# Optimization experiments

Hardware: AMD Instinct MI355X
Metric: run time of the kernel (lower is better)

The kernel has to match this reference:

```python
import jax, jax.numpy as jnp
import numpy as np

N_NODES = 50000
N_EDGES = 500000
D_NODE = 128
D_EDGE = 128
D_HID = 512
D_OUT = 128


def setup_inputs() -> dict:
    key = jax.random.key(0)
    ks = jax.random.split(key, 6)
    x = jax.random.normal(ks[0], (N_NODES, D_NODE), dtype=jnp.float32)
    edge_index = jax.random.randint(ks[1], (2, N_EDGES), 0, N_NODES, dtype=jnp.int64 if jax.config.jax_enable_x64 else jnp.int32)
    edge_attr = jax.random.normal(ks[2], (N_EDGES, D_EDGE), dtype=jnp.float32)
    cin = 2 * D_NODE + D_EDGE
    W1 = jax.random.normal(ks[3], (cin, D_HID), dtype=jnp.float32) * (1.0 / np.sqrt(cin))
    b1 = jnp.zeros((D_HID,), dtype=jnp.float32)
    W2 = jax.random.normal(ks[4], (D_HID, D_OUT), dtype=jnp.float32) * (1.0 / np.sqrt(D_HID))
    b2 = jnp.zeros((D_OUT,), dtype=jnp.float32)
    return {"x": x, "edge_index": edge_index, "edge_attr": edge_attr,
            "W1": W1, "b1": b1, "W2": W2, "b2": b2}


def reference(x, edge_index, edge_attr, W1, b1, W2, b2):
    row, col = edge_index[0], edge_index[1]
    source = x[row]            # [E, d_node] gather
    target = x[col]            # [E, d_node] gather
    out = jnp.concatenate([source, target, edge_attr], axis=1)  # [E, 2*d_node + d_edge]
    h = jax.nn.relu(out @ W1 + b1)   # [E, d_hid]
    return h @ W2 + b2               # [E, d_out]
```

## Files before the change

### kernel.cpp

```cpp
#include <hip/hip_runtime.h>

#define E_TOTAL 500000
#define N_NODES 50000
#define DN 128
#define CIN 384
#define DH 512
#define DOUT 128
#define MT 64
#define NTILE 7813
#define LDA 392
#define LDH 520

typedef short short8 __attribute__((ext_vector_type(8)));
typedef float f32x4 __attribute__((ext_vector_type(4)));

__device__ inline short f2bf(float f) {
    unsigned int u = __float_as_uint(f);
    u = (u + 0x7FFFu + ((u >> 16) & 1u)) >> 16;
    return (short)u;
}

__global__ void prep_weights(const float* __restrict__ w1,
                             const float* __restrict__ w2,
                             short* __restrict__ w1t,
                             short* __restrict__ w2t) {
    __shared__ float t[32][33];
    int b = blockIdx.x;
    const float* src; short* dst; int R, C, tr, tc;
    if (b < 192) { src = w1; dst = w1t; R = 384; C = 512; tr = b >> 4; tc = b & 15; }
    else { b -= 192; src = w2; dst = w2t; R = 512; C = 128; tr = b >> 2; tc = b & 3; }
    int lx = threadIdx.x & 31, ly = threadIdx.x >> 5;
#pragma unroll
    for (int p = 0; p < 4; p++) {
        int r = tr * 32 + p * 8 + ly;
        t[p * 8 + ly][lx] = src[(size_t)r * C + tc * 32 + lx];
    }
    __syncthreads();
#pragma unroll
    for (int p = 0; p < 4; p++) {
        int c = tc * 32 + p * 8 + ly;
        dst[(size_t)c * R + tr * 32 + lx] = f2bf(t[lx][p * 8 + ly]);
    }
}

__global__ void cvt_x(const float* __restrict__ x, short* __restrict__ xb) {
    int i = blockIdx.x * 256 + threadIdx.x;
    const float4* s = reinterpret_cast<const float4*>(x) + (size_t)i * 2;
    float4 a = s[0], b = s[1];
    short8 p;
    p[0] = f2bf(a.x); p[1] = f2bf(a.y); p[2] = f2bf(a.z); p[3] = f2bf(a.w);
    p[4] = f2bf(b.x); p[5] = f2bf(b.y); p[6] = f2bf(b.z); p[7] = f2bf(b.w);
    reinterpret_cast<short8*>(xb)[i] = p;
}

__global__ __launch_bounds__(512, 4) void edge_mlp(
        const short* __restrict__ xb,
        const float* __restrict__ xf,
        const int* __restrict__ ei,
        const float* __restrict__ ea,
        const float* __restrict__ b1,
        const float* __restrict__ b2,
        const short* __restrict__ w1t,
        const short* __restrict__ w2t,
        float* __restrict__ out) {
    __shared__ short sBuf[MT * LDH];
    __shared__ int sIdx[2][MT];
    short (*sA)[LDA] = (short (*)[LDA])sBuf;
    short (*sH)[LDH] = (short (*)[LDH])sBuf;

    const int tid = threadIdx.x;
    const int wave = tid >> 6;
    const int lane = tid & 63;
    const int l16 = lane & 15;
    const int quad = lane >> 4;
    const int lane32 = tid & 31;
    const int g = tid >> 5;
    const int e0 = blockIdx.x * MT;

    if (tid < 2 * MT) {
        int rr = tid >> 6, r = tid & 63;
        int e = e0 + r; e = e < E_TOTAL ? e : E_TOTAL - 1;
        sIdx[rr][r] = ei[rr * E_TOTAL + e];
    }
    __syncthreads();

    short4 gx[8];
    float4 ge[4];
    if (xb) {
#pragma unroll
        for (int j = 0; j < 4; j++) {
            int r = g + 16 * j;
            gx[j]     = reinterpret_cast<const short4*>(xb + (size_t)sIdx[0][r] * DN)[lane32];
            gx[4 + j] = reinterpret_cast<const short4*>(xb + (size_t)sIdx[1][r] * DN)[lane32];
            int e = e0 + r; e = e < E_TOTAL ? e : E_TOTAL - 1;
            ge[j] = reinterpret_cast<const float4*>(ea + (size_t)e * DN)[lane32];
        }
    } else {
#pragma unroll
        for (int j = 0; j < 4; j++) {
            int r = g + 16 * j;
            float4 v0 = reinterpret_cast<const float4*>(xf + (size_t)sIdx[0][r] * DN)[lane32];
            float4 v1 = reinterpret_cast<const float4*>(xf + (size_t)sIdx[1][r] * DN)[lane32];
            short4 p0, p1;
            p0.x = f2bf(v0.x); p0.y = f2bf(v0.y); p0.z = f2bf(v0.z); p0.w = f2bf(v0.w);
            p1.x = f2bf(v1.x); p1.y = f2bf(v1.y); p1.z = f2bf(v1.z); p1.w = f2bf(v1.w);
            gx[j] = p0; gx[4 + j] = p1;
            int e = e0 + r; e = e < E_TOTAL ? e : E_TOTAL - 1;
            ge[j] = reinterpret_cast<const float4*>(ea + (size_t)e * DN)[lane32];
        }
    }
    const short* base1 = w1t + (size_t)(wave * 64 + l16) * CIN + quad * 8;
    short8 bb[4];
#pragma unroll
    for (int nt = 0; nt < 4; nt++)
        bb[nt] = *reinterpret_cast<const short8*>(base1 + nt * 16 * CIN);
#pragma unroll
    for (int j = 0; j < 4; j++) {
        int r = g + 16 * j;
        *reinterpret_cast<short4*>(&sA[r][0 * DN + lane32 * 4]) = gx[j];
        *reinterpret_cast<short4*>(&sA[r][1 * DN + lane32 * 4]) = gx[4 + j];
        short4 p;
        p.x = f2bf(ge[j].x); p.y = f2bf(ge[j].y); p.z = f2bf(ge[j].z); p.w = f2bf(ge[j].w);
        *reinterpret_cast<short4*>(&sA[r][2 * DN + lane32 * 4]) = p;
    }
    __syncthreads();

    f32x4 acc[4][4] = {};
    for (int k = 0; k < CIN; k += 32) {
        short8 bn[4];
        if (k + 32 < CIN) {
#pragma unroll
            for (int nt = 0; nt < 4; nt++)
                bn[nt] = *reinterpret_cast<const short8*>(base1 + nt * 16 * CIN + k + 32);
        }
        short8 a[4];
#pragma unroll
        for (int mt = 0; mt < 4; mt++)
            a[mt] = *reinterpret_cast<const short8*>(&sA[mt * 16 + l16][k + quad * 8]);
#pragma unroll
        for (int nt = 0; nt < 4; nt++)
#pragma unroll
            for (int mt = 0; mt < 4; mt++)
                acc[nt][mt] = __builtin_amdgcn_mfma_f32_16x16x32_bf16(bb[nt], a[mt], acc[nt][mt], 0, 0, 0);
        if (k + 32 < CIN) {
#pragma unroll
            for (int nt = 0; nt < 4; nt++) bb[nt] = bn[nt];
        }
    }

    const short* base2 = w2t + (size_t)(wave * 16 + l16) * DH + quad * 8;
    short8 bw = *reinterpret_cast<const short8*>(base2);
    float4 b1v[4];
#pragma unroll
    for (int nt = 0; nt < 4; nt++)
        b1v[nt] = *reinterpret_cast<const float4*>(&b1[wave * 64 + nt * 16 + quad * 4]);

    __syncthreads();

#pragma unroll
    for (int nt = 0; nt < 4; nt++) {
#pragma unroll
        for (int mt = 0; mt < 4; mt++) {
            short4 p;
            p.x = f2bf(fmaxf(acc[nt][mt][0] + b1v[nt].x, 0.0f));
            p.y = f2bf(fmaxf(acc[nt][mt][1] + b1v[nt].y, 0.0f));
            p.z = f2bf(fmaxf(acc[nt][mt][2] + b1v[nt].z, 0.0f));
            p.w = f2bf(fmaxf(acc[nt][mt][3] + b1v[nt].w, 0.0f));
            *reinterpret_cast<short4*>(&sH[mt * 16 + l16][wave * 64 + nt * 16 + quad * 4]) = p;
        }
    }
    __syncthreads();

    f32x4 acc2[4] = {};
#pragma unroll
    for (int kk = 0; kk < 16; kk++) {
        short8 bn = bw;
        if (kk < 15) bn = *reinterpret_cast<const short8*>(base2 + (kk + 1) * 32);
        short8 hf[4];
#pragma unroll
        for (int mt = 0; mt < 4; mt++)
            hf[mt] = *reinterpret_cast<const short8*>(&sH[mt * 16 + l16][kk * 32 + quad * 8]);
#pragma unroll
        for (int mt = 0; mt < 4; mt++)
            acc2[mt] = __builtin_amdgcn_mfma_f32_16x16x32_bf16(bw, hf[mt], acc2[mt], 0, 0, 0);
        bw = bn;
    }
    float4 b2v = *reinterpret_cast<const float4*>(&b2[wave * 16 + quad * 4]);
#pragma unroll
    for (int mt = 0; mt < 4; mt++) {
        int e = e0 + mt * 16 + l16;
        if (e < E_TOTAL) {
            float4 o;
            o.x = acc2[mt][0] + b2v.x;
            o.y = acc2[mt][1] + b2v.y;
            o.z = acc2[mt][2] + b2v.z;
            o.w = acc2[mt][3] + b2v.w;
            *reinterpret_cast<float4*>(&out[(size_t)e * DOUT + wave * 16 + quad * 4]) = o;
        }
    }
}

extern "C" void kernel_launch(void* const* d_in, const int* in_sizes, int n_in,
                              void* d_out, int out_size, void* d_ws, size_t ws_size,
                              hipStream_t stream) {
    const float* x  = (const float*)d_in[0];
    const int*   ei = (const int*)d_in[1];
    const float* ea = (const float*)d_in[2];
    const float* W1 = (const float*)d_in[3];
    const float* b1 = (const float*)d_in[4];
    const float* W2 = (const float*)d_in[5];
    const float* b2 = (const float*)d_in[6];
    float* outp = (float*)d_out;

    short* w1t = (short*)d_ws;
    short* w2t = w1t + DH * CIN;
    prep_weights<<<256, 256, 0, stream>>>(W1, W2, w1t, w2t);

    const size_t wt_bytes = (size_t)(DH * CIN + DOUT * DH) * 2;
    const size_t xb_bytes = (size_t)N_NODES * DN * 2;
    short* xb = nullptr;
    if (ws_size >= wt_bytes + xb_bytes) {
        xb = w2t + DOUT * DH;
        cvt_x<<<3125, 256, 0, stream>>>(x, xb);
    }
    edge_mlp<<<NTILE, 512, 0, stream>>>(xb, x, ei, ea, b1, b2, w1t, w2t, outp);
}
```

Before: 964.1 us.

## Double edge tile to 128 with 1024 threads, XOR-swizzled LDS, staged coalesced output

Doubles the edge tile per block to 128 rows and the block to 16 waves. Each wave now owns 32 hidden columns over 128 rows in GEMM1, and in GEMM2 16 output columns over a 64-row half. This halves how often each W1 fragment is fetched from global/L2 per edge. LDS padding is replaced by an XOR swizzle to avoid bank conflicts, and results are staged through LDS so each row is written with coalesced stores. The cost is 128KB of shared memory per block, which limits occupancy to one block per CU, plus extra barriers.

New measurement: 941.7 us. 1.02x faster.

```diff
diff --git a/kernel.cpp b/kernel.cpp
--- a/kernel.cpp
+++ b/kernel.cpp
@@ -6,10 +6,11 @@
 #define CIN 384
 #define DH 512
 #define DOUT 128
-#define MT 64
-#define NTILE 7813
-#define LDA 392
-#define LDH 520
+#define MT 128
+#define NTILE 3907
+#define SA_ROWB 768
+#define SH_ROWB 1024
+#define SO_LD 132
 
 typedef short short8 __attribute__((ext_vector_type(8)));
 typedef float f32x4 __attribute__((ext_vector_type(4)));
@@ -53,7 +54,7 @@
     reinterpret_cast<short8*>(xb)[i] = p;
 }
 
-__global__ __launch_bounds__(512, 4) void edge_mlp(
+__global__ __launch_bounds__(1024, 4) void edge_mlp(
         const short* __restrict__ xb,
         const float* __restrict__ xf,
         const int* __restrict__ ei,
@@ -63,10 +64,9 @@
         const short* __restrict__ w1t,
         const short* __restrict__ w2t,
         float* __restrict__ out) {
-    __shared__ short sBuf[MT * LDH];
+    __shared__ short sBuf[65536];
     __shared__ int sIdx[2][MT];
-    short (*sA)[LDA] = (short (*)[LDA])sBuf;
-    short (*sH)[LDH] = (short (*)[LDH])sBuf;
+    char* sb = (char*)sBuf;
 
     const int tid = threadIdx.x;
     const int wave = tid >> 6;
@@ -75,10 +75,11 @@
     const int quad = lane >> 4;
     const int lane32 = tid & 31;
     const int g = tid >> 5;
+    const int xorv = (l16 & 7) << 4;
     const int e0 = blockIdx.x * MT;
 
     if (tid < 2 * MT) {
-        int rr = tid >> 6, r = tid & 63;
+        int rr = tid >> 7, r = tid & 127;
         int e = e0 + r; e = e < E_TOTAL ? e : E_TOTAL - 1;
         sIdx[rr][r] = ei[rr * E_TOTAL + e];
     }
@@ -89,7 +90,7 @@
     if (xb) {
 #pragma unroll
         for (int j = 0; j < 4; j++) {
-            int r = g + 16 * j;
+            int r = g + 32 * j;
             gx[j]     = reinterpret_cast<const short4*>(xb + (size_t)sIdx[0][r] * DN)[lane32];
             gx[4 + j] = reinterpret_cast<const short4*>(xb + (size_t)sIdx[1][r] * DN)[lane32];
             int e = e0 + r; e = e < E_TOTAL ? e : E_TOTAL - 1;
@@ -98,7 +99,7 @@
     } else {
 #pragma unroll
         for (int j = 0; j < 4; j++) {
-            int r = g + 16 * j;
+            int r = g + 32 * j;
             float4 v0 = reinterpret_cast<const float4*>(xf + (size_t)sIdx[0][r] * DN)[lane32];
             float4 v1 = reinterpret_cast<const float4*>(xf + (size_t)sIdx[1][r] * DN)[lane32];
             short4 p0, p1;
@@ -109,64 +110,72 @@
             ge[j] = reinterpret_cast<const float4*>(ea + (size_t)e * DN)[lane32];
         }
     }
-    const short* base1 = w1t + (size_t)(wave * 64 + l16) * CIN + quad * 8;
-    short8 bb[4];
-#pragma unroll
-    for (int nt = 0; nt < 4; nt++)
+    const short* base1 = w1t + (size_t)(wave * 32 + l16) * CIN + quad * 8;
+    short8 bb[2];
+#pragma unroll
+    for (int nt = 0; nt < 2; nt++)
         bb[nt] = *reinterpret_cast<const short8*>(base1 + nt * 16 * CIN);
 #pragma unroll
     for (int j = 0; j < 4; j++) {
-        int r = g + 16 * j;
-        *reinterpret_cast<short4*>(&sA[r][0 * DN + lane32 * 4]) = gx[j];
-        *reinterpret_cast<short4*>(&sA[r][1 * DN + lane32 * 4]) = gx[4 + j];
+        int r = g + 32 * j;
+        int rx = (r & 7) << 4;
+        char* row = sb + r * SA_ROWB;
+        *reinterpret_cast<short4*>(row + (( 0 * 256 + lane32 * 8) ^ rx)) = gx[j];
+        *reinterpret_cast<short4*>(row + (( 1 * 256 + lane32 * 8) ^ rx)) = gx[4 + j];
         short4 p;
         p.x = f2bf(ge[j].x); p.y = f2bf(ge[j].y); p.z = f2bf(ge[j].z); p.w = f2bf(ge[j].w);
-        *reinterpret_cast<short4*>(&sA[r][2 * DN + lane32 * 4]) = p;
-    }
-    __syncthreads();
-
-    f32x4 acc[4][4] = {};
+        *reinterpret_cast<short4*>(row + (( 2 * 256 + lane32 * 8) ^ rx)) = p;
+    }
+    __syncthreads();
+
+    f32x4 acc[2][8] = {};
     for (int k = 0; k < CIN; k += 32) {
-        short8 bn[4];
+        short8 bn[2];
         if (k + 32 < CIN) {
 #pragma unroll
-            for (int nt = 0; nt < 4; nt++)
+            for (int nt = 0; nt < 2; nt++)
                 bn[nt] = *reinterpret_cast<const short8*>(base1 + nt * 16 * CIN + k + 32);
         }
-        short8 a[4];
-#pragma unroll
-        for (int mt = 0; mt < 4; mt++)
-            a[mt] = *reinterpret_cast<const short8*>(&sA[mt * 16 + l16][k + quad * 8]);
-#pragma unroll
-        for (int nt = 0; nt < 4; nt++)
-#pragma unroll
-            for (int mt = 0; mt < 4; mt++)
+        short8 a[8];
+#pragma unroll
+        for (int mt = 0; mt < 8; mt++) {
+            int m = mt * 16 + l16;
+            a[mt] = *reinterpret_cast<const short8*>(
+                sb + m * SA_ROWB + ((2 * k + quad * 16) ^ xorv));
+        }
+#pragma unroll
+        for (int nt = 0; nt < 2; nt++)
+#pragma unroll
+            for (int mt = 0; mt < 8; mt++)
                 acc[nt][mt] = __builtin_amdgcn_mfma_f32_16x16x32_bf16(bb[nt], a[mt], acc[nt][mt], 0, 0, 0);
         if (k + 32 < CIN) {
 #pragma unroll
-            for (int nt = 0; nt < 4; nt++) bb[nt] = bn[nt];
-        }
-    }
-
-    const short* base2 = w2t + (size_t)(wave * 16 + l16) * DH + quad * 8;
+            for (int nt = 0; nt < 2; nt++) bb[nt] = bn[nt];
+        }
+    }
+
+    const int wn = wave & 7, half = wave >> 3;
+    const short* base2 = w2t + (size_t)(wn * 16 + l16) * DH + quad * 8;
     short8 bw = *reinterpret_cast<const short8*>(base2);
-    float4 b1v[4];
-#pragma unroll
-    for (int nt = 0; nt < 4; nt++)
-        b1v[nt] = *reinterpret_cast<const float4*>(&b1[wave * 64 + nt * 16 + quad * 4]);
-
-    __syncthreads();
-
-#pragma unroll
-    for (int nt = 0; nt < 4; nt++) {
-#pragma unroll
-        for (int mt = 0; mt < 4; mt++) {
+    float4 b1v[2];
+#pragma unroll
+    for (int nt = 0; nt < 2; nt++)
+        b1v[nt] = *reinterpret_cast<const float4*>(&b1[wave * 32 + nt * 16 + quad * 4]);
+
+    __syncthreads();
+
+#pragma unroll
+    for (int nt = 0; nt < 2; nt++) {
+#pragma unroll
+        for (int mt = 0; mt < 8; mt++) {
+            int m = mt * 16 + l16;
             short4 p;
             p.x = f2bf(fmaxf(acc[nt][mt][0] + b1v[nt].x, 0.0f));
             p.y = f2bf(fmaxf(acc[nt][mt][1] + b1v[nt].y, 0.0f));
             p.z = f2bf(fmaxf(acc[nt][mt][2] + b1v[nt].z, 0.0f));
             p.w = f2bf(fmaxf(acc[nt][mt][3] + b1v[nt].w, 0.0f));
-            *reinterpret_cast<short4*>(&sH[mt * 16 + l16][wave * 64 + nt * 16 + quad * 4]) = p;
+            *reinterpret_cast<short4*>(
+                sb + m * SH_ROWB + ((wave * 64 + nt * 32 + quad * 8) ^ xorv)) = p;
         }
     }
     __syncthreads();
@@ -178,24 +187,37 @@
         if (kk < 15) bn = *reinterpret_cast<const short8*>(base2 + (kk + 1) * 32);
         short8 hf[4];
 #pragma unroll
-        for (int mt = 0; mt < 4; mt++)
-            hf[mt] = *reinterpret_cast<const short8*>(&sH[mt * 16 + l16][kk * 32 + quad * 8]);
+        for (int mt = 0; mt < 4; mt++) {
+            int m = half * 64 + mt * 16 + l16;
+            hf[mt] = *reinterpret_cast<const short8*>(
+                sb + m * SH_ROWB + ((kk * 64 + quad * 16) ^ xorv));
+        }
 #pragma unroll
         for (int mt = 0; mt < 4; mt++)
             acc2[mt] = __builtin_amdgcn_mfma_f32_16x16x32_bf16(bw, hf[mt], acc2[mt], 0, 0, 0);
         bw = bn;
     }
-    float4 b2v = *reinterpret_cast<const float4*>(&b2[wave * 16 + quad * 4]);
+    float4 b2v = *reinterpret_cast<const float4*>(&b2[wn * 16 + quad * 4]);
+    __syncthreads();
+
+    float (*sO)[SO_LD] = (float (*)[SO_LD])sBuf;
 #pragma unroll
     for (int mt = 0; mt < 4; mt++) {
-        int e = e0 + mt * 16 + l16;
+        int m = half * 64 + mt * 16 + l16;
+        f32x4 o = acc2[mt];
+        float* dst = &sO[m][wn * 16 + quad * 4];
+        dst[0] = o[0] + b2v.x; dst[1] = o[1] + b2v.y;
+        dst[2] = o[2] + b2v.z; dst[3] = o[3] + b2v.w;
+    }
+    __syncthreads();
+#pragma unroll
+    for (int it = 0; it < 4; it++) {
+        int idx = tid + it * 1024;
+        int row = idx >> 5, col = (idx & 31) * 4;
+        int e = e0 + row;
         if (e < E_TOTAL) {
-            float4 o;
-            o.x = acc2[mt][0] + b2v.x;
-            o.y = acc2[mt][1] + b2v.y;
-            o.z = acc2[mt][2] + b2v.z;
-            o.w = acc2[mt][3] + b2v.w;
-            *reinterpret_cast<float4*>(&out[(size_t)e * DOUT + wave * 16 + quad * 4]) = o;
+            float4 v = *reinterpret_cast<const float4*>(&sO[row][col]);
+            *reinterpret_cast<float4*>(&out[(size_t)e * DOUT + col]) = v;
         }
     }
 }
@@ -218,10 +240,10 @@
 
     const size_t wt_bytes = (size_t)(DH * CIN + DOUT * DH) * 2;
     const size_t xb_bytes = (size_t)N_NODES * DN * 2;
-    short* xb = nullptr;
+    short* xbp = nullptr;
     if (ws_size >= wt_bytes + xb_bytes) {
-        xb = w2t + DOUT * DH;
-        cvt_x<<<3125, 256, 0, stream>>>(x, xb);
-    }
-    edge_mlp<<<NTILE, 512, 0, stream>>>(xb, x, ei, ea, b1, b2, w1t, w2t, outp);
-}
+        xbp = w2t + DOUT * DH;
+        cvt_x<<<3125, 256, 0, stream>>>(x, xbp);
+    }
+    edge_mlp<<<NTILE, 1024, 0, stream>>>(xbp, x, ei, ea, b1, b2, w1t, w2t, outp);
+}
```
